# Performance work log

Hardware: AMD Instinct MI355X
Metric: run time of the kernel (lower is better)

The kernel has to match this reference:

```python
import jax, jax.numpy as jnp
import numpy as np

E = 768
H = 8
EXP = 4
HEAD_D = E // H  # 96, also the post-softmax scaling factor


def _layernorm(x, g, b, eps=1e-5):
    mu = jnp.mean(x, axis=-1, keepdims=True)
    var = jnp.var(x, axis=-1, keepdims=True)
    return (x - mu) * jax.lax.rsqrt(var + eps) * g + b


def setup_inputs() -> dict:
    key = jax.random.key(0)
    ks = jax.random.split(key, 12)
    s = 0.02
    inp = {
        "x": jax.random.normal(ks[0], (8, 1024, E), dtype=jnp.float32),
        "ln1_g": jnp.ones((E,), jnp.float32),
        "ln1_b": jnp.zeros((E,), jnp.float32),
        "Wq": jax.random.normal(ks[1], (E, E), jnp.float32) * s,
        "bq": jnp.zeros((E,), jnp.float32),
        "Wk": jax.random.normal(ks[2], (E, E), jnp.float32) * s,
        "bk": jnp.zeros((E,), jnp.float32),
        "Wv": jax.random.normal(ks[3], (E, E), jnp.float32) * s,
        "bv": jnp.zeros((E,), jnp.float32),
        "Wo": jax.random.normal(ks[4], (E, E), jnp.float32) * s,
        "bo": jnp.zeros((E,), jnp.float32),
        "ln2_g": jnp.ones((E,), jnp.float32),
        "ln2_b": jnp.zeros((E,), jnp.float32),
        "W1": jax.random.normal(ks[5], (E, EXP * E), jnp.float32) * s,
        "b1": jnp.zeros((EXP * E,), jnp.float32),
        "W2": jax.random.normal(ks[6], (EXP * E, E), jnp.float32) * s,
        "b2": jnp.zeros((E,), jnp.float32),
    }
    return inp


def reference(x, ln1_g, ln1_b, Wq, bq, Wk, bk, Wv, bv, Wo, bo,
              ln2_g, ln2_b, W1, b1, W2, b2):
    B, N, _ = x.shape
    # --- sub_block_1: LN -> MHA (post-softmax scaling) -> residual ---
    h = _layernorm(x, ln1_g, ln1_b)
    q = (h @ Wq + bq).reshape(B, N, H, HEAD_D).transpose(0, 2, 1, 3)
    k = (h @ Wk + bk).reshape(B, N, H, HEAD_D).transpose(0, 2, 1, 3)
    v = (h @ Wv + bv).reshape(B, N, H, HEAD_D).transpose(0, 2, 1, 3)
    energy = jnp.einsum('bhqd,bhkd->bhqk', q, k)  # NOTE: no pre-softmax scale
    att = jax.nn.softmax(energy, axis=-1) * HEAD_D  # quirky post-softmax scaling
    out = jnp.einsum('bhqk,bhkd->bhqd', att, v)
    out = out.transpose(0, 2, 1, 3).reshape(B, N, E)
    out = out @ Wo + bo
    x = x + out  # residual
    # --- sub_block_2: LN -> GELU-FFN (NO residual, faithful to source) ---
    h = _layernorm(x, ln2_g, ln2_b)
    h = jax.nn.gelu(h @ W1 + b1, approximate=False)
    return h @ W2 + b2
```

## Files before the change

kernel.cpp:

```cpp
#include <hip/hip_runtime.h>
#include <hip/hip_bf16.h>
#include <math.h>

#define DI __device__ __forceinline__

typedef __attribute__((ext_vector_type(8))) __bf16 bf16x8;
typedef __attribute__((ext_vector_type(8))) short short8;
typedef __attribute__((ext_vector_type(4))) float f32x4;
typedef __attribute__((ext_vector_type(4))) int int4v;
typedef __attribute__((ext_vector_type(4))) unsigned short ushort4v;

DI short f2bfn(float f) {
  __bf16 b = (__bf16)f;
  short s;
  __builtin_memcpy(&s, &b, 2);
  return s;
}

DI void gload_lds16(const void* g, void* l) {
  __builtin_amdgcn_global_load_lds(
      (const __attribute__((address_space(1))) void*)g,
      (__attribute__((address_space(3))) void*)l, 16, 0, 0);
}

__global__ __launch_bounds__(256) void transpose_cvt(
    const float* __restrict__ in, short* __restrict__ out, int K, int N)
{
  __shared__ float tile[32][33];
  const int tx = threadIdx.x & 31, ty = threadIdx.x >> 5;
  const int n0 = blockIdx.x * 32, k0 = blockIdx.y * 32;
#pragma unroll
  for (int p = 0; p < 4; ++p)
    tile[ty + p * 8][tx] = in[(size_t)(k0 + ty + p * 8) * N + n0 + tx];
  __syncthreads();
#pragma unroll
  for (int p = 0; p < 4; ++p)
    out[(size_t)(n0 + ty + p * 8) * K + k0 + tx] = f2bfn(tile[tx][ty + p * 8]);
}

__global__ __launch_bounds__(256) void v_transpose(
    const short* __restrict__ qkv, short* __restrict__ vT)
{
  __shared__ short tile[64][98];
  const int t = threadIdx.x;
  const int bh = blockIdx.x, nt = blockIdx.y;
  const int b = bh >> 3, h = bh & 7;
  const size_t gbase = (size_t)(b * 1024 + nt * 64) * 2304 + 1536 + h * 96;
#pragma unroll
  for (int i = 0; i < 3; ++i) {
    const int p = i * 256 + t;
    const int row = p / 12, cb = p % 12;
    const short8 v = *(const short8*)(qkv + gbase + (size_t)row * 2304 + cb * 8);
#pragma unroll
    for (int j = 0; j < 4; ++j) {
      unsigned pk = (unsigned)(unsigned short)v[2 * j] |
                    ((unsigned)(unsigned short)v[2 * j + 1] << 16);
      *(unsigned*)&tile[row][cb * 8 + 2 * j] = pk;
    }
  }
  __syncthreads();
#pragma unroll
  for (int i = 0; i < 3; ++i) {
    const int p = i * 256 + t;
    const int d = p >> 3, cb = p & 7;
    short8 o;
#pragma unroll
    for (int j = 0; j < 8; ++j) o[j] = tile[cb * 8 + j][d];
    *(short8*)(vT + ((size_t)bh * 96 + d) * 1024 + nt * 64 + cb * 8) = o;
  }
}

__global__ __launch_bounds__(256) void ln_rows(
    const float* __restrict__ x, const float* __restrict__ gw,
    const float* __restrict__ bw, unsigned short* __restrict__ out)
{
  const int wv = threadIdx.x >> 6, ln = threadIdx.x & 63;
  const size_t row = (size_t)blockIdx.x * 4 + wv;
  const float* xr = x + row * 768;
  float4 v[3];
  float s = 0.f, sq = 0.f;
#pragma unroll
  for (int i = 0; i < 3; ++i) {
    v[i] = *(const float4*)(xr + i * 256 + ln * 4);
    s  += v[i].x + v[i].y + v[i].z + v[i].w;
    sq += v[i].x * v[i].x + v[i].y * v[i].y + v[i].z * v[i].z + v[i].w * v[i].w;
  }
#pragma unroll
  for (int msk = 1; msk < 64; msk <<= 1) {
    s  += __shfl_xor(s, msk);
    sq += __shfl_xor(sq, msk);
  }
  const float mean = s * (1.f / 768.f);
  const float var  = sq * (1.f / 768.f) - mean * mean;
  const float rstd = rsqrtf(var + 1e-5f);
#pragma unroll
  for (int i = 0; i < 3; ++i) {
    const int c = i * 256 + ln * 4;
    const float vals[4] = {v[i].x, v[i].y, v[i].z, v[i].w};
    ushort4v o;
#pragma unroll
    for (int j = 0; j < 4; ++j)
      o[j] = (unsigned short)f2bfn((vals[j] - mean) * rstd * gw[c + j] + bw[c + j]);
    *(ushort4v*)(out + row * 768 + c) = o;
  }
}

enum { EPI_BF16 = 0, EPI_F32_RES = 1, EPI_BF16_GELU = 2, EPI_F32 = 3 };
#define EPITCH 132

template <int MODE, int BM, int BK, int MW>
__global__ __launch_bounds__(256, MW) void gemm_bt(
    const short* __restrict__ A,
    const short* __restrict__ Bt,
    const float* __restrict__ bias,
    const float* __restrict__ resid,
    void* __restrict__ Cout, int ldc,
    int Ntiles, int K)
{
  constexpr int NCHUNK = BK / 8;
  constexpr int CMASK = NCHUNK - 1;
  constexpr int ABYTES = BM * BK * 2;
  constexpr int STAGE_BYTES = (BM + 128) * BK * 2;
  constexpr int NLA = BM * BK / 8 / 256;
  constexpr int NLB = 128 * BK / 8 / 256;
  constexpr int LOADS = NLA + NLB;
  constexpr int MR = BM / 32;
  constexpr int NKK = BK / 32;
  constexpr int SMEM = 2 * STAGE_BYTES > 32 * EPITCH * 4 ? 2 * STAGE_BYTES
                                                         : 32 * EPITCH * 4;
  __shared__ __align__(16) char smem[SMEM];
  const int t = threadIdx.x;
  const int wv = t >> 6, ln = t & 63;
  const int g = ln >> 4, r = ln & 15;
  const int sw = ((int)blockIdx.x & 7) * ((int)gridDim.x >> 3) + ((int)blockIdx.x >> 3);
  const int bm = sw / Ntiles, bn = sw % Ntiles;
  const int wr = wv >> 1, wc = wv & 1;
  f32x4 acc[MR][4] = {};

  const char* aptr[NLA];
  const char* bptr[NLB];
#pragma unroll
  for (int q = 0; q < NLA; ++q) {
    const int p = q * 256 + t;
    const int row = p / NCHUNK, c = (p & CMASK) ^ (row & CMASK);
    aptr[q] = (const char*)(A + (size_t)(bm * BM + row) * K + c * 8);
  }
#pragma unroll
  for (int q = 0; q < NLB; ++q) {
    const int p = q * 256 + t;
    const int row = p / NCHUNK, c = (p & CMASK) ^ (row & CMASK);
    bptr[q] = (const char*)(Bt + (size_t)(bn * 128 + row) * K + c * 8);
  }

  auto stage = [&](int buf) {
    char* as = smem + buf * STAGE_BYTES;
    char* bs = as + ABYTES;
#pragma unroll
    for (int q = 0; q < NLA; ++q) {
      gload_lds16(aptr[q], as + q * 4096 + wv * 1024);
      aptr[q] += BK * 2;
    }
#pragma unroll
    for (int q = 0; q < NLB; ++q) {
      gload_lds16(bptr[q], bs + q * 4096 + wv * 1024);
      bptr[q] += BK * 2;
    }
  };

  const int nk = K / BK;
  stage(0);
  stage(1);
  int cur = 0;
  for (int kt = 0; kt < nk; ++kt) {
    if (kt + 1 < nk)
      asm volatile("s_waitcnt vmcnt(%0)\n\ts_barrier" :: "n"(LOADS) : "memory");
    else
      asm volatile("s_waitcnt vmcnt(0)\n\ts_barrier" ::: "memory");
    const short* as = (const short*)(smem + cur * STAGE_BYTES);
    const short* bs = as + ABYTES / 2;
    bf16x8 af[MR][NKK], bfr[4][NKK];
#pragma unroll
    for (int m = 0; m < MR; ++m) {
      const int row = wr * (BM / 2) + m * 16 + r;
#pragma unroll
      for (int kk = 0; kk < NKK; ++kk)
        af[m][kk] = *(const bf16x8*)(as + row * BK + (((kk * 4 + g) ^ (row & CMASK)) << 3));
    }
#pragma unroll
    for (int n = 0; n < 4; ++n) {
      const int row = wc * 64 + n * 16 + r;
#pragma unroll
      for (int kk = 0; kk < NKK; ++kk)
        bfr[n][kk] = *(const bf16x8*)(bs + row * BK + (((kk * 4 + g) ^ (row & CMASK)) << 3));
    }
#pragma unroll
    for (int kk = 0; kk < NKK; ++kk)
#pragma unroll
      for (int m = 0; m < MR; ++m)
#pragma unroll
        for (int n = 0; n < 4; ++n)
          acc[m][n] = __builtin_amdgcn_mfma_f32_16x16x32_bf16(af[m][kk], bfr[n][kk],
                                                              acc[m][n], 0, 0, 0);
    if (kt + 2 < nk) {
      asm volatile("s_waitcnt lgkmcnt(0)\n\ts_barrier" ::: "memory");
      stage(cur);
    }
    cur ^= 1;
  }
  __syncthreads();

  float* epi = (float*)smem;
  const int cq = (t & 7) * 16;
  const int c0 = bn * 128 + cq;
  f32x4 bv[4];
#pragma unroll
  for (int j = 0; j < 4; ++j) bv[j] = *(const f32x4*)(bias + c0 + j * 4);

#pragma unroll
  for (int m = 0; m < MR; ++m) {
#pragma unroll
    for (int n = 0; n < 4; ++n) {
      const int col = wc * 64 + n * 16 + r;
#pragma unroll
      for (int q = 0; q < 4; ++q)
        epi[(wr * 16 + g * 4 + q) * EPITCH + col] = acc[m][n][q];
    }
    __syncthreads();
    const int lr = t >> 3;
    const size_t grow = (size_t)(bm * BM + (lr < 16 ? m * 16 + lr
                                                    : BM / 2 + m * 16 + (lr - 16)));
    float vals[16];
#pragma unroll
    for (int j = 0; j < 4; ++j) {
      const f32x4 vv = *(const f32x4*)(epi + lr * EPITCH + cq + j * 4);
#pragma unroll
      for (int e = 0; e < 4; ++e) vals[j * 4 + e] = vv[e] + bv[j][e];
    }
    if constexpr (MODE == EPI_F32_RES) {
#pragma unroll
      for (int j = 0; j < 4; ++j) {
        const f32x4 rv = *(const f32x4*)(resid + grow * ldc + c0 + j * 4);
#pragma unroll
        for (int e = 0; e < 4; ++e) vals[j * 4 + e] += rv[e];
      }
    }
    if constexpr (MODE == EPI_BF16_GELU) {
#pragma unroll
      for (int j = 0; j < 16; ++j)
        vals[j] = 0.5f * vals[j] * (1.0f + erff(vals[j] * 0.70710678118654752f));
    }
    if constexpr (MODE == EPI_F32 || MODE == EPI_F32_RES) {
      float* op = (float*)Cout + grow * ldc + c0;
#pragma unroll
      for (int j = 0; j < 4; ++j) {
        f32x4 ov;
#pragma unroll
        for (int e = 0; e < 4; ++e) ov[e] = vals[j * 4 + e];
        *(f32x4*)(op + j * 4) = ov;
      }
    } else {
      unsigned short* op = (unsigned short*)Cout + grow * ldc + c0;
#pragma unroll
      for (int hhalf = 0; hhalf < 2; ++hhalf) {
        short8 ov;
#pragma unroll
        for (int e = 0; e < 8; ++e) ov[e] = f2bfn(vals[hhalf * 8 + e]);
        *(short8*)(op + hhalf * 8) = ov;
      }
    }
    __syncthreads();
  }
}

__global__ __launch_bounds__(256, 2) void attn_fwd(
    const short* __restrict__ qkv, const short* __restrict__ vT,
    unsigned short* __restrict__ ab)
{
  __shared__ short Ks[2][64 * 128];
  __shared__ short Vs[2][96 * 64];
  __shared__ short Ps[4][2][16 * 64];
  const int t = threadIdx.x, wv = t >> 6, ln = t & 63;
  const int g = ln >> 4, r = ln & 15;
  const int bid = ((int)blockIdx.x & 7) * 64 + ((int)blockIdx.x >> 3);
  const int bh = bid >> 3, qt = bid & 7;
  const int b = bh >> 3, h = bh & 7;

  bf16x8 qf[2][3];
#pragma unroll
  for (int u = 0; u < 2; ++u) {
    const size_t rowq = (size_t)(b * 1024 + qt * 128 + wv * 32 + u * 16 + r);
#pragma unroll
    for (int kd = 0; kd < 3; ++kd)
      qf[u][kd] = *(const bf16x8*)(qkv + rowq * 2304 + h * 96 + kd * 32 + g * 8);
  }

  size_t offK[4];
#pragma unroll
  for (int i = 0; i < 4; ++i) {
    const int p = i * 256 + t;
    const int row = p >> 4, cb = p & 15, cbs = cb ^ (row & 7);
    offK[i] = (size_t)row * 2304 + 768 + h * 96 + (cbs << 3);
  }
  size_t offV[3];
#pragma unroll
  for (int i = 0; i < 3; ++i) {
    const int p = i * 256 + t;
    const int row = p >> 3, cb = p & 7, cbs = cb ^ (row & 7);
    offV[i] = ((size_t)bh * 96 + row) * 1024 + (cbs << 3);
  }
  const short* qb = qkv + (size_t)b * 1024 * 2304;

  auto stageKV = [&](int buf, int kt) {
    const size_t kadd = (size_t)kt * 64 * 2304;
#pragma unroll
    for (int i = 0; i < 4; ++i)
      gload_lds16(qb + kadd + offK[i], (char*)Ks[buf] + i * 4096 + wv * 1024);
#pragma unroll
    for (int i = 0; i < 3; ++i)
      gload_lds16(vT + offV[i] + kt * 64, (char*)Vs[buf] + i * 4096 + wv * 1024);
  };

  f32x4 o[2][6] = {};
  float mr[2] = {-1e30f, -1e30f}, lr[2] = {0.f, 0.f};

  stageKV(0, 0);
  __syncthreads();
  int cur = 0;
  for (int kt = 0; kt < 16; ++kt) {
    if (kt < 15) stageKV(cur ^ 1, kt + 1);
    const short* ks = Ks[cur];
    const short* vs = Vs[cur];

    f32x4 s[2][4] = {};
    __builtin_amdgcn_s_setprio(1);
#pragma unroll
    for (int sub = 0; sub < 4; ++sub) {
      bf16x8 kf[3];
#pragma unroll
      for (int kd = 0; kd < 3; ++kd)
        kf[kd] = *(const bf16x8*)(
            ks + (sub * 16 + r) * 128 + (((kd * 4 + g) ^ (r & 7)) << 3));
#pragma unroll
      for (int u = 0; u < 2; ++u)
#pragma unroll
        for (int kd = 0; kd < 3; ++kd)
          s[u][sub] = __builtin_amdgcn_mfma_f32_16x16x32_bf16(kf[kd], qf[u][kd],
                                                              s[u][sub], 0, 0, 0);
    }
    __builtin_amdgcn_s_setprio(0);

#pragma unroll
    for (int u = 0; u < 2; ++u) {
      float tm = fmaxf(fmaxf(s[u][0][0], s[u][0][1]),
                       fmaxf(s[u][0][2], s[u][0][3]));
#pragma unroll
      for (int sub = 1; sub < 4; ++sub)
        tm = fmaxf(tm, fmaxf(fmaxf(s[u][sub][0], s[u][sub][1]),
                             fmaxf(s[u][sub][2], s[u][sub][3])));
      tm = fmaxf(tm, __shfl_xor(tm, 16));
      tm = fmaxf(tm, __shfl_xor(tm, 32));

      if (__any(tm > mr[u] + 8.f)) {
        const float mnew = fmaxf(mr[u], tm);
        const float sc = __expf(mr[u] - mnew);
        lr[u] *= sc;
        mr[u] = mnew;
        float scr[4];
#pragma unroll
        for (int reg = 0; reg < 4; ++reg)
          scr[reg] = __shfl(sc, (ln & 48) | (g * 4 + reg));
#pragma unroll
        for (int nd = 0; nd < 6; ++nd)
#pragma unroll
          for (int reg = 0; reg < 4; ++reg) o[u][nd][reg] *= scr[reg];
      }

      float tsum = 0.f;
#pragma unroll
      for (int sub = 0; sub < 4; ++sub) {
        float p0 = __expf(s[u][sub][0] - mr[u]);
        float p1 = __expf(s[u][sub][1] - mr[u]);
        float p2 = __expf(s[u][sub][2] - mr[u]);
        float p3 = __expf(s[u][sub][3] - mr[u]);
        tsum += (p0 + p1) + (p2 + p3);
        ushort4v pk;
        pk[0] = (unsigned short)f2bfn(p0);
        pk[1] = (unsigned short)f2bfn(p1);
        pk[2] = (unsigned short)f2bfn(p2);
        pk[3] = (unsigned short)f2bfn(p3);
        const int c8 = (sub * 4 + g) ^ ((r & 7) << 1);
        *(ushort4v*)((char*)Ps[wv][u] + r * 128 + c8 * 8) = pk;
      }
      tsum += __shfl_xor(tsum, 16);
      tsum += __shfl_xor(tsum, 32);
      lr[u] += tsum;
    }

    bf16x8 pf[2][2];
#pragma unroll
    for (int u = 0; u < 2; ++u)
#pragma unroll
      for (int kk = 0; kk < 2; ++kk)
        pf[u][kk] = *(const bf16x8*)(
            Ps[wv][u] + r * 64 + (((kk * 4 + g) ^ (r & 7)) << 3));
    __builtin_amdgcn_s_setprio(1);
#pragma unroll
    for (int nd = 0; nd < 6; ++nd) {
      bf16x8 vf[2];
#pragma unroll
      for (int kk = 0; kk < 2; ++kk)
        vf[kk] = *(const bf16x8*)(
            vs + (nd * 16 + r) * 64 + (((kk * 4 + g) ^ (r & 7)) << 3));
#pragma unroll
      for (int u = 0; u < 2; ++u)
#pragma unroll
        for (int kk = 0; kk < 2; ++kk)
          o[u][nd] = __builtin_amdgcn_mfma_f32_16x16x32_bf16(pf[u][kk], vf[kk],
                                                             o[u][nd], 0, 0, 0);
    }
    __builtin_amdgcn_s_setprio(0);

    __syncthreads();
    cur ^= 1;
  }

#pragma unroll
  for (int u = 0; u < 2; ++u) {
    float linv[4];
#pragma unroll
    for (int reg = 0; reg < 4; ++reg)
      linv[reg] = 96.0f / __shfl(lr[u], (ln & 48) | (g * 4 + reg));
#pragma unroll
    for (int reg = 0; reg < 4; ++reg) {
      const size_t row = (size_t)(b * 1024 + qt * 128 + wv * 32 + u * 16 + g * 4 + reg);
#pragma unroll
      for (int nd = 0; nd < 6; ++nd)
        ab[row * 768 + h * 96 + nd * 16 + r] =
            (unsigned short)f2bfn(o[u][nd][reg] * linv[reg]);
    }
  }
}

extern "C" void kernel_launch(void* const* d_in, const int* in_sizes, int n_in,
                              void* d_out, int out_size, void* d_ws, size_t ws_size,
                              hipStream_t stream)
{
  const float* x    = (const float*)d_in[0];
  const float* ln1g = (const float*)d_in[1];
  const float* ln1b = (const float*)d_in[2];
  const float* Wq   = (const float*)d_in[3];
  const float* bq   = (const float*)d_in[4];
  const float* Wk   = (const float*)d_in[5];
  const float* bk   = (const float*)d_in[6];
  const float* Wv   = (const float*)d_in[7];
  const float* bv   = (const float*)d_in[8];
  const float* Wo   = (const float*)d_in[9];
  const float* bo   = (const float*)d_in[10];
  const float* ln2g = (const float*)d_in[11];
  const float* ln2b = (const float*)d_in[12];
  const float* W1   = (const float*)d_in[13];
  const float* b1   = (const float*)d_in[14];
  const float* W2   = (const float*)d_in[15];
  const float* b2   = (const float*)d_in[16];

  char* ws = (char*)d_ws;
  size_t off = 0;
  short* Wtqkv = (short*)(ws + off); off += (size_t)2304 * 768 * 2;
  short* Wto   = (short*)(ws + off); off += (size_t)768 * 768 * 2;
  short* Wt1   = (short*)(ws + off); off += (size_t)3072 * 768 * 2;
  short* Wt2   = (short*)(ws + off); off += (size_t)768 * 3072 * 2;
  float* bqkv  = (float*)(ws + off); off += 16384;
  short* hb    = (short*)(ws + off); off += (size_t)8192 * 768 * 2;
  short* qkv   = (short*)(ws + off); off += (size_t)8192 * 2304 * 2;
  short* h2b   = (short*)(ws + off); off += (size_t)8192 * 768 * 2;
  short* f1 = hb;
  short* ab = hb;
  short* vT = h2b;
  float* x1 = (float*)d_out;

  transpose_cvt<<<dim3(24, 24), 256, 0, stream>>>(Wq, Wtqkv, 768, 768);
  transpose_cvt<<<dim3(24, 24), 256, 0, stream>>>(Wk, Wtqkv + (size_t)768 * 768, 768, 768);
  transpose_cvt<<<dim3(24, 24), 256, 0, stream>>>(Wv, Wtqkv + (size_t)1536 * 768, 768, 768);
  transpose_cvt<<<dim3(24, 24), 256, 0, stream>>>(Wo, Wto, 768, 768);
  transpose_cvt<<<dim3(96, 24), 256, 0, stream>>>(W1, Wt1, 768, 3072);
  transpose_cvt<<<dim3(24, 96), 256, 0, stream>>>(W2, Wt2, 3072, 768);
  hipMemcpyAsync(bqkv,        bq, 768 * sizeof(float), hipMemcpyDeviceToDevice, stream);
  hipMemcpyAsync(bqkv + 768,  bk, 768 * sizeof(float), hipMemcpyDeviceToDevice, stream);
  hipMemcpyAsync(bqkv + 1536, bv, 768 * sizeof(float), hipMemcpyDeviceToDevice, stream);

  ln_rows<<<2048, 256, 0, stream>>>(x, ln1g, ln1b, (unsigned short*)hb);
  gemm_bt<EPI_BF16, 128, 32, 4><<<64 * 18, 256, 0, stream>>>(hb, Wtqkv, bqkv, nullptr, qkv, 2304, 18, 768);
  v_transpose<<<dim3(64, 16), 256, 0, stream>>>(qkv, vT);
  attn_fwd<<<512, 256, 0, stream>>>(qkv, vT, (unsigned short*)ab);
  gemm_bt<EPI_F32_RES, 64, 64, 3><<<128 * 6, 256, 0, stream>>>(ab, Wto, bo, x, x1, 768, 6, 768);

  ln_rows<<<2048, 256, 0, stream>>>(x1, ln2g, ln2b, (unsigned short*)h2b);
  gemm_bt<EPI_BF16_GELU, 128, 32, 4><<<64 * 24, 256, 0, stream>>>(h2b, Wt1, b1, nullptr, f1, 3072, 24, 768);
  gemm_bt<EPI_F32, 64, 64, 3><<<128 * 6, 256, 0, stream>>>(f1, Wt2, b2, nullptr, (float*)d_out, 768, 6, 3072);
}
```

Measured before the change: 264.4 us.

## Use per-wave epilogue staging without block barriers and a fast erf for GELU

```diff
diff --git a/kernel.cpp b/kernel.cpp
--- a/kernel.cpp
+++ b/kernel.cpp
@@ -15,6 +15,19 @@
   short s;
   __builtin_memcpy(&s, &b, 2);
   return s;
+}
+
+DI float erf_fast(float x) {
+  const float ax = fabsf(x);
+  const float t = __builtin_amdgcn_rcpf(1.0f + 0.3275911f * ax);
+  float p = 1.061405429f;
+  p = p * t - 1.453152027f;
+  p = p * t + 1.421413741f;
+  p = p * t - 0.284496736f;
+  p = p * t + 0.254829592f;
+  p = p * t;
+  const float r = 1.0f - p * __expf(-ax * ax);
+  return copysignf(r, x);
 }
 
 DI void gload_lds16(const void* g, void* l) {
@@ -106,7 +119,6 @@
 }
 
 enum { EPI_BF16 = 0, EPI_F32_RES = 1, EPI_BF16_GELU = 2, EPI_F32 = 3 };
-#define EPITCH 132
 
 template <int MODE, int BM, int BK, int MW>
 __global__ __launch_bounds__(256, MW) void gemm_bt(
@@ -126,8 +138,7 @@
   constexpr int LOADS = NLA + NLB;
   constexpr int MR = BM / 32;
   constexpr int NKK = BK / 32;
-  constexpr int SMEM = 2 * STAGE_BYTES > 32 * EPITCH * 4 ? 2 * STAGE_BYTES
-                                                         : 32 * EPITCH * 4;
+  constexpr int SMEM = 2 * STAGE_BYTES > 4 * 4352 ? 2 * STAGE_BYTES : 4 * 4352;
   __shared__ __align__(16) char smem[SMEM];
   const int t = threadIdx.x;
   const int wv = t >> 6, ln = t & 63;
@@ -209,9 +220,10 @@
   }
   __syncthreads();
 
-  float* epi = (float*)smem;
-  const int cq = (t & 7) * 16;
-  const int c0 = bn * 128 + cq;
+  float* epi = (float*)(smem + wv * 4352);
+  const int cq = (ln & 3) * 16;
+  const int lr = ln >> 2;
+  const int c0 = bn * 128 + wc * 64 + cq;
   f32x4 bv[4];
 #pragma unroll
   for (int j = 0; j < 4; ++j) bv[j] = *(const f32x4*)(bias + c0 + j * 4);
@@ -219,20 +231,15 @@
 #pragma unroll
   for (int m = 0; m < MR; ++m) {
 #pragma unroll
-    for (int n = 0; n < 4; ++n) {
-      const int col = wc * 64 + n * 16 + r;
+    for (int n = 0; n < 4; ++n)
 #pragma unroll
       for (int q = 0; q < 4; ++q)
-        epi[(wr * 16 + g * 4 + q) * EPITCH + col] = acc[m][n][q];
-    }
-    __syncthreads();
-    const int lr = t >> 3;
-    const size_t grow = (size_t)(bm * BM + (lr < 16 ? m * 16 + lr
-                                                    : BM / 2 + m * 16 + (lr - 16)));
+        epi[(g * 4 + q) * 68 + n * 16 + r] = acc[m][n][q];
+    const size_t grow = (size_t)(bm * BM + wr * (BM / 2) + m * 16 + lr);
     float vals[16];
 #pragma unroll
     for (int j = 0; j < 4; ++j) {
-      const f32x4 vv = *(const f32x4*)(epi + lr * EPITCH + cq + j * 4);
+      const f32x4 vv = *(const f32x4*)(epi + lr * 68 + cq + j * 4);
 #pragma unroll
       for (int e = 0; e < 4; ++e) vals[j * 4 + e] = vv[e] + bv[j][e];
     }
@@ -247,7 +254,7 @@
     if constexpr (MODE == EPI_BF16_GELU) {
 #pragma unroll
       for (int j = 0; j < 16; ++j)
-        vals[j] = 0.5f * vals[j] * (1.0f + erff(vals[j] * 0.70710678118654752f));
+        vals[j] = 0.5f * vals[j] * (1.0f + erf_fast(vals[j] * 0.70710678118654752f));
     }
     if constexpr (MODE == EPI_F32 || MODE == EPI_F32_RES) {
       float* op = (float*)Cout + grow * ldc + c0;
@@ -268,7 +275,6 @@
         *(short8*)(op + hhalf * 8) = ov;
       }
     }
-    __syncthreads();
   }
 }
 
```

New measurement: 262.9 us. Within noise of the previous version (-0.6%).
